# Kernel optimization log

Measured on AMD Instinct MI355X. Metric: run time of the kernel, lower is better.

The kernel has to match this reference:

```python
import jax, jax.numpy as jnp
import numpy as np

IN_SIZE = 5        # per-segment features: [number, In, former_number, speed0, speed1]
HIDDEN = 128
OUT_HIDDEN = 128
OUT_SIZE = 3       # input_size = output_size + 2 (structural constraint)
T_PREDICT = 4
B, T, S = 8, 128, 128


def setup_inputs() -> dict:
    key = jax.random.key(0)
    ks = jax.random.split(key, 5)
    scale = 0.05
    return {
        "input_data": jax.random.normal(ks[0], (B, T, S, IN_SIZE), jnp.float32),
        # seg_model: fused LSTM weight over concat(x, h, h_after, h_before)
        "W_cell": jax.random.normal(ks[1], (IN_SIZE + 3 * HIDDEN, 4 * HIDDEN), jnp.float32) * scale,
        "b_cell": jnp.zeros((4 * HIDDEN,), jnp.float32),
        # FCNet layerSize=[hidden, output_hidden, output]: Linear-ReLU-Linear
        "W1": jax.random.normal(ks[2], (HIDDEN, OUT_HIDDEN), jnp.float32) * scale,
        "b1": jnp.zeros((OUT_HIDDEN,), jnp.float32),
        "W2": jax.random.normal(ks[3], (OUT_HIDDEN, OUT_SIZE), jnp.float32) * scale,
        "b2": jnp.zeros((OUT_SIZE,), jnp.float32),
    }


def _cell(x, h, c, h_after, h_before, W, b):
    # LSTM cell on concat(x, h, h_after, h_before): [B,S,IN+3H] @ [IN+3H,4H]
    z = jnp.concatenate([x, h, h_after, h_before], axis=-1) @ W + b
    i, f, g, o = jnp.split(z, 4, axis=-1)
    c_new = jax.nn.sigmoid(f) * c + jax.nn.sigmoid(i) * jnp.tanh(g)
    h_new = jax.nn.sigmoid(o) * jnp.tanh(c_new)
    return h_new, c_new


def _next_input(former_input, next_input, output):
    # faithful translation of caculate_next_input
    speed_output = output[:, 1:, 1:]                    # [B,S-1,OUT-1]
    number_output = output[:, :, 0:1]                   # [B,S,1]
    speed_input = next_input[:, 0:1, 3:]                # [B,1,IN-3]
    In = jnp.concatenate([next_input[:, 0:1, 1:2], number_output[:, :-1, :]], axis=1)
    former_number = former_input[:, :, 2:3]
    number_caculate = former_number + In - number_output
    speed_next = jnp.concatenate([speed_input, speed_output], axis=1)
    return jnp.concatenate([number_output, In, number_caculate, speed_next], axis=2)


def reference(input_data, W_cell, b_cell, W1, b1, W2, b2):
    b, t, s, f = input_data.shape
    # time-major inputs for scan: x at time k and time k+1
    x_t = jnp.transpose(input_data[:, :-1], (1, 0, 2, 3))   # [T-1,B,S,F]
    x_tp1 = jnp.transpose(input_data[:, 1:], (1, 0, 2, 3))  # [T-1,B,S,F]
    h0 = jnp.zeros((b, s, HIDDEN), input_data.dtype)
    c0 = jnp.zeros((b, s, HIDDEN), input_data.dtype)

    def step(carry, xs):
        h, c = carry
        xt, xn = xs
        # spatial neighbor shift: h_after[i] = h[i+1], h_before[i] = h[i-1]
        h_after = jnp.pad(h[:, 1:, :], ((0, 0), (0, 1), (0, 0)))
        h_before = jnp.pad(h[:, :-1, :], ((0, 0), (1, 0), (0, 0)))
        h, c = _cell(xt, h, c, h_after, h_before, W_cell, b_cell)
        out = jnp.maximum(h @ W1 + b1, 0.0) @ W2 + b2
        nd = _next_input(xt, xn, out)
        return (h, c), nd

    _, nds = jax.lax.scan(step, (h0, c0), (x_t, x_tp1))     # [T-1,B,S,F]
    # original only writes outputs for time >= t_predict
    outputs = jnp.transpose(nds[T_PREDICT:], (1, 0, 2, 3))  # [B,T-TP-1,S,F]
    return outputs
```

## Files before the change

kernel.cpp:

```cpp
#include <hip/hip_runtime.h>
#include <hip/hip_bf16.h>


#define NB 8
#define NT 128
#define NS 128
#define NSTEP 127
#define TPRED 4
#define TOUT 123

typedef __attribute__((ext_vector_type(4))) float f32x4;
typedef __attribute__((ext_vector_type(8))) short s16x8;
typedef __attribute__((ext_vector_type(4))) unsigned int u32x4;

#define WS_WTC 0
#define WS_WT1 (512*384*2)
#define WS_PUB (WS_WT1 + 128*128*2)
#define WS_PUB_BYTES (2*8*8*2*128*4)

#define BARRIER() do { \
    __builtin_amdgcn_sched_barrier(0); \
    asm volatile("s_waitcnt lgkmcnt(0)" ::: "memory"); \
    __builtin_amdgcn_s_barrier(); \
    __builtin_amdgcn_sched_barrier(0); \
} while (0)

__device__ __forceinline__ unsigned swz(unsigned off) {
    return off ^ (((off >> 8) & 7u) << 4);
}

__global__ void init_weights(const float* __restrict__ Wc, const float* __restrict__ W1,
                             __hip_bfloat16* __restrict__ WTc, __hip_bfloat16* __restrict__ WT1)
{
    int i = blockIdx.x * blockDim.x + threadIdx.x;
    if (i < 512*384) {
        int cpp = i / 384, k = i % 384;
        int q = cpp >> 6, rem = cpp & 63, g = rem >> 4, h = rem & 15;
        int oc = g*128 + 16*q + h;
        int row = (k < 128) ? (261 + k) : ((k < 256) ? (5 + (k - 128)) : (133 + (k - 256)));
        WTc[cpp*384 + k] = __float2bfloat16(Wc[row*512 + oc]);
    } else {
        int qq = i - 512*384;
        if (qq < 128*128) {
            int nn = qq >> 7, k = qq & 127;
            WT1[nn*128 + k] = __float2bfloat16(W1[k*128 + nn]);
        }
    }
}

__global__ __launch_bounds__(512, 1) void lstm_persist(
    const float* __restrict__ input, const float* __restrict__ Wc,
    const float* __restrict__ bc, const float* __restrict__ b1v,
    const float* __restrict__ W2, const float* __restrict__ b2,
    float* __restrict__ outp,
    const __hip_bfloat16* __restrict__ WTc, const __hip_bfloat16* __restrict__ WT1,
    unsigned* pub)
{
    __shared__ __align__(16) __hip_bfloat16 hl[2*18*128];
    __shared__ __align__(16) __hip_bfloat16 relu_l[18*128];
    __shared__ float xl[3][80];
    __shared__ float outl[17*3];
    __shared__ float w2l[3*128];
    __shared__ float b2l[3];

    const int tid  = threadIdx.x;
    const int blk  = blockIdx.x;
    const int b    = blk & 7;
    const int c    = blk >> 3;
    const int lane = tid & 63;
    const int w    = tid >> 6;
    const int arow = lane & 15;
    const int kgrp = lane >> 4;
    const int hidw = 16*w + arow;

    for (int i = tid; i < 2*18*128; i += 512) ((unsigned short*)hl)[i] = 0;
    if (tid < 384) w2l[tid] = W2[(tid & 127)*3 + (tid >> 7)];
    if (tid >= 384 && tid < 387) b2l[tid - 384] = b2[tid - 384];

    float wxr[4][5], bcr[4];
    #pragma unroll
    for (int g = 0; g < 4; ++g) {
        const int cg = g*128 + hidw;
        bcr[g] = bc[cg];
        #pragma unroll
        for (int f = 0; f < 5; ++f) wxr[g][f] = Wc[f*512 + cg];
    }
    const float b1r = b1v[hidw];

    s16x8 brg[4][12];
    #pragma unroll
    for (int g = 0; g < 4; ++g)
        #pragma unroll
        for (int kt = 0; kt < 12; ++kt)
            brg[g][kt] = *(const s16x8*)((const char*)WTc +
                ((unsigned)(w*64 + g*16 + arow)*384 + kt*32 + kgrp*8)*2);
    s16x8 w1r[4];
    #pragma unroll
    for (int kt = 0; kt < 4; ++kt)
        w1r[kt] = *(const s16x8*)((const char*)WT1 + ((unsigned)(hidw)*128 + kt*32 + kgrp*8)*2);

    float cst[4] = {0.f, 0.f, 0.f, 0.f};

    if (tid < 80) xl[0][tid] = input[((unsigned)(b*NT)*NS + 16*c)*5 + tid];

    __syncthreads();

    for (int j = 0; j <= NSTEP; ++j) {
        const int jm3 = j % 3;
        const unsigned hlb  = (unsigned)(j & 1) * 4608u;
        const unsigned nhlb = (unsigned)((j + 1) & 1) * 4608u;

        if (j > 0 && tid < 64) {
            const bool left = (tid < 32);
            if (left ? (c > 0) : (c < 7)) {
                const unsigned jt = (unsigned)j;
                const int nc   = left ? (c - 1) : (c + 1);
                const int side = left ? 1 : 0;
                const int col4 = (tid & 31) * 4;
                const unsigned* q = pub + (unsigned)(((j & 1)*8 + b)*8 + nc)*256 + side*128 + col4;
                u32x4 g;
                for (;;) {
                    asm volatile("global_load_dwordx4 %0, %1, off sc0 sc1\n\ts_waitcnt vmcnt(0)"
                                 : "=v"(g) : "v"(q) : "memory");
                    if ((g[0] >> 16) == jt && (g[1] >> 16) == jt &&
                        (g[2] >> 16) == jt && (g[3] >> 16) == jt) break;
                }
                __builtin_amdgcn_sched_barrier(0);
                const unsigned long long pk =
                    (unsigned long long)(g[0] & 0xffffu)        |
                    ((unsigned long long)(g[1] & 0xffffu) << 16) |
                    ((unsigned long long)(g[2] & 0xffffu) << 32) |
                    ((unsigned long long)(g[3] & 0xffffu) << 48);
                const int row = left ? 0 : 17;
                *(unsigned long long*)((char*)hl + hlb + swz((unsigned)(row*256 + col4*2))) = pk;
            }
        }
        float xr = 0.f;
        const bool xact = (j < NSTEP) && (tid < 80);
        if (xact) xr = input[((unsigned)(b*NT + j + 1)*NS + 16*c)*5 + tid];

        BARRIER();

        if (j < NSTEP) {
            f32x4 a0 = {0.f,0.f,0.f,0.f}, a1 = a0, a2 = a0, a3 = a0;
            const unsigned ab = (unsigned)(arow*256 + kgrp*16);
            #pragma unroll
            for (int kt = 0; kt < 4; ++kt) {
                const s16x8 av = *(const s16x8*)((const char*)hl + hlb + swz(ab + kt*64));
                a0 = __builtin_amdgcn_mfma_f32_16x16x32_bf16(av, brg[0][kt], a0, 0, 0, 0);
                a1 = __builtin_amdgcn_mfma_f32_16x16x32_bf16(av, brg[1][kt], a1, 0, 0, 0);
                a2 = __builtin_amdgcn_mfma_f32_16x16x32_bf16(av, brg[2][kt], a2, 0, 0, 0);
                a3 = __builtin_amdgcn_mfma_f32_16x16x32_bf16(av, brg[3][kt], a3, 0, 0, 0);
            }
            #pragma unroll
            for (int kt = 4; kt < 8; ++kt) {
                const s16x8 av = *(const s16x8*)((const char*)hl + hlb + swz(ab + 256 + (kt-4)*64));
                a0 = __builtin_amdgcn_mfma_f32_16x16x32_bf16(av, brg[0][kt], a0, 0, 0, 0);
                a1 = __builtin_amdgcn_mfma_f32_16x16x32_bf16(av, brg[1][kt], a1, 0, 0, 0);
                a2 = __builtin_amdgcn_mfma_f32_16x16x32_bf16(av, brg[2][kt], a2, 0, 0, 0);
                a3 = __builtin_amdgcn_mfma_f32_16x16x32_bf16(av, brg[3][kt], a3, 0, 0, 0);
            }
            #pragma unroll
            for (int kt = 8; kt < 12; ++kt) {
                const s16x8 av = *(const s16x8*)((const char*)hl + hlb + swz(ab + 512 + (kt-8)*64));
                a0 = __builtin_amdgcn_mfma_f32_16x16x32_bf16(av, brg[0][kt], a0, 0, 0, 0);
                a1 = __builtin_amdgcn_mfma_f32_16x16x32_bf16(av, brg[1][kt], a1, 0, 0, 0);
                a2 = __builtin_amdgcn_mfma_f32_16x16x32_bf16(av, brg[2][kt], a2, 0, 0, 0);
                a3 = __builtin_amdgcn_mfma_f32_16x16x32_bf16(av, brg[3][kt], a3, 0, 0, 0);
            }
            asm volatile("s_waitcnt vmcnt(0)" ::: "memory");
            unsigned short h0b = 0, h3b = 0;
            #pragma unroll
            for (int r = 0; r < 4; ++r) {
                const int lr0 = kgrp*4 + r;
                const float xv0 = xl[jm3][lr0*5+0], xv1 = xl[jm3][lr0*5+1], xv2 = xl[jm3][lr0*5+2],
                            xv3 = xl[jm3][lr0*5+3], xv4 = xl[jm3][lr0*5+4];
                const float iv = a0[r] + bcr[0] + xv0*wxr[0][0] + xv1*wxr[0][1] + xv2*wxr[0][2] + xv3*wxr[0][3] + xv4*wxr[0][4];
                const float fv = a1[r] + bcr[1] + xv0*wxr[1][0] + xv1*wxr[1][1] + xv2*wxr[1][2] + xv3*wxr[1][3] + xv4*wxr[1][4];
                const float gv = a2[r] + bcr[2] + xv0*wxr[2][0] + xv1*wxr[2][1] + xv2*wxr[2][2] + xv3*wxr[2][3] + xv4*wxr[2][4];
                const float ov = a3[r] + bcr[3] + xv0*wxr[3][0] + xv1*wxr[3][1] + xv2*wxr[3][2] + xv3*wxr[3][3] + xv4*wxr[3][4];
                const float si = __builtin_amdgcn_rcpf(1.f + __expf(-iv));
                const float sf = __builtin_amdgcn_rcpf(1.f + __expf(-fv));
                const float so = __builtin_amdgcn_rcpf(1.f + __expf(-ov));
                const float tg = 1.f - 2.f*__builtin_amdgcn_rcpf(__expf(2.f*gv) + 1.f);
                const float cn = sf*cst[r] + si*tg;
                cst[r] = cn;
                const float tc = 1.f - 2.f*__builtin_amdgcn_rcpf(__expf(2.f*cn) + 1.f);
                const float hn = so*tc;
                __hip_bfloat16 hbv = __float2bfloat16(hn);
                const unsigned short hbits = *(const unsigned short*)&hbv;
                *(unsigned short*)((char*)hl + nhlb + swz((unsigned)((lr0 + 1)*256 + hidw*2))) = hbits;
                if (r == 0) h0b = hbits;
                if (r == 3) h3b = hbits;
            }
            unsigned* pbase = pub + (unsigned)((((j+1) & 1)*8 + b)*8 + c)*256;
            const unsigned jt1 = (unsigned)(j + 1) << 16;
            if (c > 0 && kgrp == 0)
                asm volatile("global_store_dword %0, %1, off sc0 sc1"
                             :: "v"(pbase + hidw), "v"(jt1 | (unsigned)h0b) : "memory");
            if (c < 7 && kgrp == 3)
                asm volatile("global_store_dword %0, %1, off sc0 sc1"
                             :: "v"(pbase + 128 + hidw), "v"(jt1 | (unsigned)h3b) : "memory");
        }

        if (j >= TPRED + 1) {
            const int jm1_3 = (j - 1) % 3;
            f32x4 c0 = {0.f,0.f,0.f,0.f}, c1 = c0;
            const unsigned w1a = (unsigned)(arow*256 + kgrp*16);
            #pragma unroll
            for (int kt = 0; kt < 4; ++kt) {
                const s16x8 av0 = *(const s16x8*)((const char*)hl + hlb + swz(w1a + kt*64));
                const s16x8 av1 = *(const s16x8*)((const char*)hl + hlb + swz(w1a + 256 + kt*64));
                c0 = __builtin_amdgcn_mfma_f32_16x16x32_bf16(av0, w1r[kt], c0, 0, 0, 0);
                c1 = __builtin_amdgcn_mfma_f32_16x16x32_bf16(av1, w1r[kt], c1, 0, 0, 0);
            }
            #pragma unroll
            for (int r = 0; r < 4; ++r) {
                const int lr = kgrp*4 + r;
                const float v0 = fmaxf(c0[r] + b1r, 0.f);
                *(__hip_bfloat16*)((char*)relu_l + swz((unsigned)(lr*256 + hidw*2))) = __float2bfloat16(v0);
                if (lr == 15) {
                    const float v1 = fmaxf(c1[r] + b1r, 0.f);
                    *(__hip_bfloat16*)((char*)relu_l + swz((unsigned)(16*256 + hidw*2))) = __float2bfloat16(v1);
                }
            }
            BARRIER();
            if (tid < 51) {
                const int m = tid / 3, p = tid - m*3;
                float s = b2l[p];
                #pragma unroll
                for (int kc = 0; kc < 16; ++kc) {
                    union { s16x8 v; unsigned short u[8]; } uu;
                    uu.v = *(const s16x8*)((const char*)relu_l + swz((unsigned)(m*256 + kc*16)));
                    #pragma unroll
                    for (int e = 0; e < 8; ++e)
                        s += __uint_as_float((unsigned)uu.u[e] << 16) * w2l[p*128 + kc*8 + e];
                }
                outl[m*3 + p] = s;
            }
            if (tid < 16) {
                const int m = tid, grow = 16*c + m;
                const float no = outl[(m + 1)*3 + 0];
                float In, sp0, sp1;
                if (m == 0 && c == 0) { In = xl[jm3][1]; sp0 = xl[jm3][3]; sp1 = xl[jm3][4]; }
                else { In = outl[m*3 + 0]; sp0 = outl[(m + 1)*3 + 1]; sp1 = outl[(m + 1)*3 + 2]; }
                const float former = xl[jm1_3][m*5 + 2];
                const long base = ((long)(b*TOUT + (j - 1 - TPRED))*NS + grow)*5;
                outp[base + 0] = no;
                outp[base + 1] = In;
                outp[base + 2] = former + In - no;
                outp[base + 3] = sp0;
                outp[base + 4] = sp1;
            }
        }

        if (xact) xl[(j + 1) % 3][tid] = xr;
    }
}

extern "C" void kernel_launch(void* const* d_in, const int* in_sizes, int n_in,
                              void* d_out, int out_size, void* d_ws, size_t ws_size,
                              hipStream_t stream) {
    const float* input = (const float*)d_in[0];
    const float* Wc    = (const float*)d_in[1];
    const float* bc    = (const float*)d_in[2];
    const float* W1    = (const float*)d_in[3];
    const float* b1    = (const float*)d_in[4];
    const float* W2    = (const float*)d_in[5];
    const float* b2    = (const float*)d_in[6];
    float* outp = (float*)d_out;
    char* ws = (char*)d_ws;

    __hip_bfloat16* WTc = (__hip_bfloat16*)(ws + WS_WTC);
    __hip_bfloat16* WT1 = (__hip_bfloat16*)(ws + WS_WT1);
    unsigned*       pub = (unsigned*)(ws + WS_PUB);

    hipMemsetAsync(ws + WS_PUB, 0, WS_PUB_BYTES, stream);
    init_weights<<<832, 256, 0, stream>>>(Wc, W1, WTc, WT1);
    lstm_persist<<<64, 512, 0, stream>>>(input, Wc, bc, b1, W2, b2, outp, WTc, WT1, pub);
}
```

Baseline: 1.003 ms.

## Exchange halos every 8 steps using 8-row ghost zones with redundant compute

Each block now computes 32 rows per step: its own 16 plus 8 ghost rows on each side. Neighbour h and c state is exchanged through global memory only every 8 steps instead of every step. The input projection and bias are folded into the MFMA as extra K columns, fed from a bf16 input tile with a ones column and weights held in LDS. This trades double the MFMA and gate work per step for far fewer inter-block spin-waits, and it adds LDS pressure.

```diff
diff --git a/kernel.cpp b/kernel.cpp
--- a/kernel.cpp
+++ b/kernel.cpp
@@ -14,9 +14,9 @@
 typedef __attribute__((ext_vector_type(4))) unsigned int u32x4;
 
 #define WS_WTC 0
-#define WS_WT1 (512*384*2)
-#define WS_PUB (WS_WT1 + 128*128*2)
-#define WS_PUB_BYTES (2*8*8*2*128*4)
+#define WS_WT1 (512*416*2)
+#define WS_HCP (WS_WT1 + 128*128*2)
+#define WS_HCP_BYTES (2*8*8*2*8*128*8)
 
 #define BARRIER() do { \
     __builtin_amdgcn_sched_barrier(0); \
@@ -29,35 +29,41 @@
     return off ^ (((off >> 8) & 7u) << 4);
 }
 
-__global__ void init_weights(const float* __restrict__ Wc, const float* __restrict__ W1,
+__global__ void init_weights(const float* __restrict__ Wc, const float* __restrict__ bc,
+                             const float* __restrict__ W1,
                              __hip_bfloat16* __restrict__ WTc, __hip_bfloat16* __restrict__ WT1)
 {
     int i = blockIdx.x * blockDim.x + threadIdx.x;
-    if (i < 512*384) {
-        int cpp = i / 384, k = i % 384;
+    if (i < 512*416) {
+        int cpp = i / 416, k = i % 416;
         int q = cpp >> 6, rem = cpp & 63, g = rem >> 4, h = rem & 15;
         int oc = g*128 + 16*q + h;
-        int row = (k < 128) ? (261 + k) : ((k < 256) ? (5 + (k - 128)) : (133 + (k - 256)));
-        WTc[cpp*384 + k] = __float2bfloat16(Wc[row*512 + oc]);
-    } else {
-        int qq = i - 512*384;
-        if (qq < 128*128) {
-            int nn = qq >> 7, k = qq & 127;
-            WT1[nn*128 + k] = __float2bfloat16(W1[k*128 + nn]);
-        }
+        float v;
+        if      (k < 128) v = Wc[(261 + k)*512 + oc];
+        else if (k < 256) v = Wc[(5 + (k - 128))*512 + oc];
+        else if (k < 384) v = Wc[(133 + (k - 256))*512 + oc];
+        else if (k < 389) v = Wc[(k - 384)*512 + oc];
+        else if (k == 389) v = bc[oc];
+        else v = 0.f;
+        WTc[cpp*416 + k] = __float2bfloat16(v);
+    } else if (i < 512*416 + 128*128) {
+        int qq = i - 512*416;
+        int nn = qq >> 7, k = qq & 127;
+        WT1[nn*128 + k] = __float2bfloat16(W1[k*128 + nn]);
     }
 }
 
 __global__ __launch_bounds__(512, 1) void lstm_persist(
-    const float* __restrict__ input, const float* __restrict__ Wc,
-    const float* __restrict__ bc, const float* __restrict__ b1v,
+    const float* __restrict__ input, const float* __restrict__ b1v,
     const float* __restrict__ W2, const float* __restrict__ b2,
     float* __restrict__ outp,
     const __hip_bfloat16* __restrict__ WTc, const __hip_bfloat16* __restrict__ WT1,
-    unsigned* pub)
+    unsigned long long* hcpub)
 {
-    __shared__ __align__(16) __hip_bfloat16 hl[2*18*128];
+    __shared__ __align__(16) __hip_bfloat16 hl[2*34*128];
+    __shared__ __align__(16) __hip_bfloat16 bl[512*104];
     __shared__ __align__(16) __hip_bfloat16 relu_l[18*128];
+    __shared__ __align__(16) __hip_bfloat16 xlt[2*32*40];
     __shared__ float xl[3][80];
     __shared__ float outl[17*3];
     __shared__ float w2l[3*128];
@@ -67,146 +73,237 @@
     const int blk  = blockIdx.x;
     const int b    = blk & 7;
     const int c    = blk >> 3;
+    const int s0   = 16*c;
     const int lane = tid & 63;
-    const int w    = tid >> 6;
+    const int q    = tid >> 6;
     const int arow = lane & 15;
     const int kgrp = lane >> 4;
-    const int hidw = 16*w + arow;
-
-    for (int i = tid; i < 2*18*128; i += 512) ((unsigned short*)hl)[i] = 0;
+    const int hidw = 16*q + arow;
+
+    for (int i = tid; i < 2*34*128; i += 512) ((unsigned short*)hl)[i] = 0;
+    for (int i = tid; i < 2*32*40; i += 512) ((unsigned short*)xlt)[i] = 0;
     if (tid < 384) w2l[tid] = W2[(tid & 127)*3 + (tid >> 7)];
     if (tid >= 384 && tid < 387) b2l[tid - 384] = b2[tid - 384];
-
-    float wxr[4][5], bcr[4];
-    #pragma unroll
-    for (int g = 0; g < 4; ++g) {
-        const int cg = g*128 + hidw;
-        bcr[g] = bc[cg];
-        #pragma unroll
-        for (int f = 0; f < 5; ++f) wxr[g][f] = Wc[f*512 + cg];
+    for (int i = tid; i < 512*24; i += 512) {
+        const int col = i / 24, r8 = i % 24;
+        const int kt = 10 + (r8 >> 3), sub = r8 & 7;
+        *(unsigned long long*)((char*)bl + col*208 + (kt - 10)*64 + sub*8) =
+            *(const unsigned long long*)((const char*)WTc + ((unsigned)col*416 + kt*32 + sub*4)*2);
     }
-    const float b1r = b1v[hidw];
-
-    s16x8 brg[4][12];
+    if (tid < 80) xl[0][tid] = input[((unsigned)(b*NT)*NS + s0)*5 + tid];
+    if (tid < 32) {
+        int g = s0 - 8 + tid; g = g < 0 ? 0 : (g > 127 ? 127 : g);
+        const float* xp = input + ((unsigned)(b*NT)*NS + g)*5;
+        unsigned short* xr0 = (unsigned short*)((char*)xlt + tid*80);
+        __hip_bfloat16 v0 = __float2bfloat16(xp[0]), v1 = __float2bfloat16(xp[1]),
+                       v2 = __float2bfloat16(xp[2]), v3 = __float2bfloat16(xp[3]),
+                       v4 = __float2bfloat16(xp[4]);
+        xr0[0] = *(unsigned short*)&v0; xr0[1] = *(unsigned short*)&v1;
+        xr0[2] = *(unsigned short*)&v2; xr0[3] = *(unsigned short*)&v3;
+        xr0[4] = *(unsigned short*)&v4; xr0[5] = 0x3F80;
+    }
+
+    s16x8 brg[4][10];
     #pragma unroll
     for (int g = 0; g < 4; ++g)
         #pragma unroll
-        for (int kt = 0; kt < 12; ++kt)
+        for (int kt = 0; kt < 10; ++kt)
             brg[g][kt] = *(const s16x8*)((const char*)WTc +
-                ((unsigned)(w*64 + g*16 + arow)*384 + kt*32 + kgrp*8)*2);
+                ((unsigned)(q*64 + g*16 + arow)*416 + kt*32 + kgrp*8)*2);
     s16x8 w1r[4];
     #pragma unroll
     for (int kt = 0; kt < 4; ++kt)
-        w1r[kt] = *(const s16x8*)((const char*)WT1 + ((unsigned)(hidw)*128 + kt*32 + kgrp*8)*2);
-
-    float cst[4] = {0.f, 0.f, 0.f, 0.f};
-
-    if (tid < 80) xl[0][tid] = input[((unsigned)(b*NT)*NS + 16*c)*5 + tid];
+        w1r[kt] = *(const s16x8*)((const char*)WT1 + ((unsigned)hidw*128 + kt*32 + kgrp*8)*2);
+    const float b1r = b1v[hidw];
+
+    float cst[8];
+    #pragma unroll
+    for (int i = 0; i < 8; ++i) cst[i] = 0.f;
 
     __syncthreads();
 
     for (int j = 0; j <= NSTEP; ++j) {
         const int jm3 = j % 3;
-        const unsigned hlb  = (unsigned)(j & 1) * 4608u;
-        const unsigned nhlb = (unsigned)((j + 1) & 1) * 4608u;
-
-        if (j > 0 && tid < 64) {
-            const bool left = (tid < 32);
-            if (left ? (c > 0) : (c < 7)) {
-                const unsigned jt = (unsigned)j;
-                const int nc   = left ? (c - 1) : (c + 1);
-                const int side = left ? 1 : 0;
-                const int col4 = (tid & 31) * 4;
-                const unsigned* q = pub + (unsigned)(((j & 1)*8 + b)*8 + nc)*256 + side*128 + col4;
-                u32x4 g;
+        const unsigned hlb  = (unsigned)(j & 1) * 8704u;
+        const unsigned nhlb = (unsigned)((j + 1) & 1) * 8704u;
+        const unsigned xlb  = (unsigned)(j & 1) * 2560u;
+
+        float xr = 0.f, p0 = 0.f, p1 = 0.f, p2 = 0.f, p3 = 0.f, p4 = 0.f;
+        const bool act80 = (j < NSTEP) && (tid < 80);
+        const bool act32 = (j < NSTEP) && (tid < 32);
+        if (act80) xr = input[((unsigned)(b*NT + j + 1)*NS + s0)*5 + tid];
+        if (act32) {
+            int g = s0 - 8 + tid; g = g < 0 ? 0 : (g > 127 ? 127 : g);
+            const float* xp = input + ((unsigned)(b*NT + j + 1)*NS + g)*5;
+            p0 = xp[0]; p1 = xp[1]; p2 = xp[2]; p3 = xp[3]; p4 = xp[4];
+        }
+
+        const bool isgather = (j > 0) && ((j & 7) == 0);
+        if (isgather) {
+            const unsigned wtag = (unsigned)(j >> 3);
+            const unsigned par  = wtag & 1;
+            const int side = tid >> 8;
+            const int i2   = tid & 255;
+            const bool act = (side == 0) ? (c > 0) : (c < 7);
+            if (act) {
+                const int nc = (side == 0) ? c - 1 : c + 1;
+                const int ns = 1 - side;
+                const unsigned long long* qp =
+                    hcpub + (unsigned)((((par*8 + b)*8 + nc)*2 + ns)*1024 + i2*4);
+                u32x4 ga, gb;
                 for (;;) {
-                    asm volatile("global_load_dwordx4 %0, %1, off sc0 sc1\n\ts_waitcnt vmcnt(0)"
-                                 : "=v"(g) : "v"(q) : "memory");
-                    if ((g[0] >> 16) == jt && (g[1] >> 16) == jt &&
-                        (g[2] >> 16) == jt && (g[3] >> 16) == jt) break;
+                    asm volatile(
+                        "global_load_dwordx4 %0, %2, off sc0 sc1\n\t"
+                        "global_load_dwordx4 %1, %3, off sc0 sc1\n\t"
+                        "s_waitcnt vmcnt(0)"
+                        : "=&v"(ga), "=&v"(gb)
+                        : "v"(qp), "v"(qp + 2) : "memory");
+                    if ((ga[1] >> 16) == wtag && (ga[3] >> 16) == wtag &&
+                        (gb[1] >> 16) == wtag && (gb[3] >> 16) == wtag) break;
                 }
                 __builtin_amdgcn_sched_barrier(0);
+                const int row = i2 >> 5, col0 = (i2 & 31)*4;
+                const int lr = (side == 0) ? 1 + row : 25 + row;
                 const unsigned long long pk =
-                    (unsigned long long)(g[0] & 0xffffu)        |
-                    ((unsigned long long)(g[1] & 0xffffu) << 16) |
-                    ((unsigned long long)(g[2] & 0xffffu) << 32) |
-                    ((unsigned long long)(g[3] & 0xffffu) << 48);
-                const int row = left ? 0 : 17;
-                *(unsigned long long*)((char*)hl + hlb + swz((unsigned)(row*256 + col4*2))) = pk;
-            }
-        }
-        float xr = 0.f;
-        const bool xact = (j < NSTEP) && (tid < 80);
-        if (xact) xr = input[((unsigned)(b*NT + j + 1)*NS + 16*c)*5 + tid];
-
+                    (unsigned long long)(ga[1] & 0xffffu)
+                  | ((unsigned long long)(ga[3] & 0xffffu) << 16)
+                  | ((unsigned long long)(gb[1] & 0xffffu) << 32)
+                  | ((unsigned long long)(gb[3] & 0xffffu) << 48);
+                *(unsigned long long*)((char*)hl + hlb + swz((unsigned)(lr*256 + col0*2))) = pk;
+            }
+            BARRIER();
+            if (c > 0 && kgrp < 2) {
+                const unsigned long long* cp =
+                    hcpub + (unsigned)((((par*8 + b)*8 + (c - 1))*2 + 1)*1024 + (kgrp*4)*128 + hidw);
+                unsigned long long v0, v1, v2, v3;
+                asm volatile(
+                    "global_load_dwordx2 %0, %4, off sc0 sc1\n\t"
+                    "global_load_dwordx2 %1, %5, off sc0 sc1\n\t"
+                    "global_load_dwordx2 %2, %6, off sc0 sc1\n\t"
+                    "global_load_dwordx2 %3, %7, off sc0 sc1\n\t"
+                    "s_waitcnt vmcnt(0)"
+                    : "=&v"(v0), "=&v"(v1), "=&v"(v2), "=&v"(v3)
+                    : "v"(cp), "v"(cp + 128), "v"(cp + 256), "v"(cp + 384) : "memory");
+                cst[0] = __uint_as_float((unsigned)v0);
+                cst[1] = __uint_as_float((unsigned)v1);
+                cst[2] = __uint_as_float((unsigned)v2);
+                cst[3] = __uint_as_float((unsigned)v3);
+            }
+            if (c < 7 && kgrp >= 2) {
+                const unsigned long long* cp =
+                    hcpub + (unsigned)((((par*8 + b)*8 + (c + 1))*2 + 0)*1024 + ((kgrp - 2)*4)*128 + hidw);
+                unsigned long long v0, v1, v2, v3;
+                asm volatile(
+                    "global_load_dwordx2 %0, %4, off sc0 sc1\n\t"
+                    "global_load_dwordx2 %1, %5, off sc0 sc1\n\t"
+                    "global_load_dwordx2 %2, %6, off sc0 sc1\n\t"
+                    "global_load_dwordx2 %3, %7, off sc0 sc1\n\t"
+                    "s_waitcnt vmcnt(0)"
+                    : "=&v"(v0), "=&v"(v1), "=&v"(v2), "=&v"(v3)
+                    : "v"(cp), "v"(cp + 128), "v"(cp + 256), "v"(cp + 384) : "memory");
+                cst[4] = __uint_as_float((unsigned)v0);
+                cst[5] = __uint_as_float((unsigned)v1);
+                cst[6] = __uint_as_float((unsigned)v2);
+                cst[7] = __uint_as_float((unsigned)v3);
+            }
+        }
         BARRIER();
 
         if (j < NSTEP) {
-            f32x4 a0 = {0.f,0.f,0.f,0.f}, a1 = a0, a2 = a0, a3 = a0;
-            const unsigned ab = (unsigned)(arow*256 + kgrp*16);
+            const bool PUB = ((j + 1) & 7) == 0;
+            const unsigned wtag1 = (unsigned)((j + 1) >> 3);
+            unsigned hsv[4], csv[4];
             #pragma unroll
-            for (int kt = 0; kt < 4; ++kt) {
-                const s16x8 av = *(const s16x8*)((const char*)hl + hlb + swz(ab + kt*64));
-                a0 = __builtin_amdgcn_mfma_f32_16x16x32_bf16(av, brg[0][kt], a0, 0, 0, 0);
-                a1 = __builtin_amdgcn_mfma_f32_16x16x32_bf16(av, brg[1][kt], a1, 0, 0, 0);
-                a2 = __builtin_amdgcn_mfma_f32_16x16x32_bf16(av, brg[2][kt], a2, 0, 0, 0);
-                a3 = __builtin_amdgcn_mfma_f32_16x16x32_bf16(av, brg[3][kt], a3, 0, 0, 0);
-            }
-            #pragma unroll
-            for (int kt = 4; kt < 8; ++kt) {
-                const s16x8 av = *(const s16x8*)((const char*)hl + hlb + swz(ab + 256 + (kt-4)*64));
-                a0 = __builtin_amdgcn_mfma_f32_16x16x32_bf16(av, brg[0][kt], a0, 0, 0, 0);
-                a1 = __builtin_amdgcn_mfma_f32_16x16x32_bf16(av, brg[1][kt], a1, 0, 0, 0);
-                a2 = __builtin_amdgcn_mfma_f32_16x16x32_bf16(av, brg[2][kt], a2, 0, 0, 0);
-                a3 = __builtin_amdgcn_mfma_f32_16x16x32_bf16(av, brg[3][kt], a3, 0, 0, 0);
-            }
-            #pragma unroll
-            for (int kt = 8; kt < 12; ++kt) {
-                const s16x8 av = *(const s16x8*)((const char*)hl + hlb + swz(ab + 512 + (kt-8)*64));
-                a0 = __builtin_amdgcn_mfma_f32_16x16x32_bf16(av, brg[0][kt], a0, 0, 0, 0);
-                a1 = __builtin_amdgcn_mfma_f32_16x16x32_bf16(av, brg[1][kt], a1, 0, 0, 0);
-                a2 = __builtin_amdgcn_mfma_f32_16x16x32_bf16(av, brg[2][kt], a2, 0, 0, 0);
-                a3 = __builtin_amdgcn_mfma_f32_16x16x32_bf16(av, brg[3][kt], a3, 0, 0, 0);
-            }
-            asm volatile("s_waitcnt vmcnt(0)" ::: "memory");
-            unsigned short h0b = 0, h3b = 0;
-            #pragma unroll
-            for (int r = 0; r < 4; ++r) {
-                const int lr0 = kgrp*4 + r;
-                const float xv0 = xl[jm3][lr0*5+0], xv1 = xl[jm3][lr0*5+1], xv2 = xl[jm3][lr0*5+2],
-                            xv3 = xl[jm3][lr0*5+3], xv4 = xl[jm3][lr0*5+4];
-                const float iv = a0[r] + bcr[0] + xv0*wxr[0][0] + xv1*wxr[0][1] + xv2*wxr[0][2] + xv3*wxr[0][3] + xv4*wxr[0][4];
-                const float fv = a1[r] + bcr[1] + xv0*wxr[1][0] + xv1*wxr[1][1] + xv2*wxr[1][2] + xv3*wxr[1][3] + xv4*wxr[1][4];
-                const float gv = a2[r] + bcr[2] + xv0*wxr[2][0] + xv1*wxr[2][1] + xv2*wxr[2][2] + xv3*wxr[2][3] + xv4*wxr[2][4];
-                const float ov = a3[r] + bcr[3] + xv0*wxr[3][0] + xv1*wxr[3][1] + xv2*wxr[3][2] + xv3*wxr[3][3] + xv4*wxr[3][4];
-                const float si = __builtin_amdgcn_rcpf(1.f + __expf(-iv));
-                const float sf = __builtin_amdgcn_rcpf(1.f + __expf(-fv));
-                const float so = __builtin_amdgcn_rcpf(1.f + __expf(-ov));
-                const float tg = 1.f - 2.f*__builtin_amdgcn_rcpf(__expf(2.f*gv) + 1.f);
-                const float cn = sf*cst[r] + si*tg;
-                cst[r] = cn;
-                const float tc = 1.f - 2.f*__builtin_amdgcn_rcpf(__expf(2.f*cn) + 1.f);
-                const float hn = so*tc;
-                __hip_bfloat16 hbv = __float2bfloat16(hn);
-                const unsigned short hbits = *(const unsigned short*)&hbv;
-                *(unsigned short*)((char*)hl + nhlb + swz((unsigned)((lr0 + 1)*256 + hidw*2))) = hbits;
-                if (r == 0) h0b = hbits;
-                if (r == 3) h3b = hbits;
-            }
-            unsigned* pbase = pub + (unsigned)((((j+1) & 1)*8 + b)*8 + c)*256;
-            const unsigned jt1 = (unsigned)(j + 1) << 16;
-            if (c > 0 && kgrp == 0)
-                asm volatile("global_store_dword %0, %1, off sc0 sc1"
-                             :: "v"(pbase + hidw), "v"(jt1 | (unsigned)h0b) : "memory");
-            if (c < 7 && kgrp == 3)
-                asm volatile("global_store_dword %0, %1, off sc0 sc1"
-                             :: "v"(pbase + 128 + hidw), "v"(jt1 | (unsigned)h3b) : "memory");
+            for (int mt = 0; mt < 2; ++mt) {
+                f32x4 a0 = {0.f,0.f,0.f,0.f}, a1 = a0, a2 = a0, a3 = a0;
+                const unsigned ab = (unsigned)((mt*16 + arow)*256 + kgrp*16);
+                #pragma unroll
+                for (int kt = 0; kt < 4; ++kt) {
+                    const s16x8 av = *(const s16x8*)((const char*)hl + hlb + swz(ab + kt*64));
+                    a0 = __builtin_amdgcn_mfma_f32_16x16x32_bf16(av, brg[0][kt], a0, 0, 0, 0);
+                    a1 = __builtin_amdgcn_mfma_f32_16x16x32_bf16(av, brg[1][kt], a1, 0, 0, 0);
+                    a2 = __builtin_amdgcn_mfma_f32_16x16x32_bf16(av, brg[2][kt], a2, 0, 0, 0);
+                    a3 = __builtin_amdgcn_mfma_f32_16x16x32_bf16(av, brg[3][kt], a3, 0, 0, 0);
+                }
+                #pragma unroll
+                for (int kt = 4; kt < 8; ++kt) {
+                    const s16x8 av = *(const s16x8*)((const char*)hl + hlb + swz(ab + 256 + (kt-4)*64));
+                    a0 = __builtin_amdgcn_mfma_f32_16x16x32_bf16(av, brg[0][kt], a0, 0, 0, 0);
+                    a1 = __builtin_amdgcn_mfma_f32_16x16x32_bf16(av, brg[1][kt], a1, 0, 0, 0);
+                    a2 = __builtin_amdgcn_mfma_f32_16x16x32_bf16(av, brg[2][kt], a2, 0, 0, 0);
+                    a3 = __builtin_amdgcn_mfma_f32_16x16x32_bf16(av, brg[3][kt], a3, 0, 0, 0);
+                }
+                #pragma unroll
+                for (int kt = 8; kt < 10; ++kt) {
+                    const s16x8 av = *(const s16x8*)((const char*)hl + hlb + swz(ab + 512 + (kt-8)*64));
+                    a0 = __builtin_amdgcn_mfma_f32_16x16x32_bf16(av, brg[0][kt], a0, 0, 0, 0);
+                    a1 = __builtin_amdgcn_mfma_f32_16x16x32_bf16(av, brg[1][kt], a1, 0, 0, 0);
+                    a2 = __builtin_amdgcn_mfma_f32_16x16x32_bf16(av, brg[2][kt], a2, 0, 0, 0);
+                    a3 = __builtin_amdgcn_mfma_f32_16x16x32_bf16(av, brg[3][kt], a3, 0, 0, 0);
+                }
+                #pragma unroll
+                for (int kt = 10; kt < 12; ++kt) {
+                    const s16x8 av = *(const s16x8*)((const char*)hl + hlb + swz(ab + 512 + (kt-8)*64));
+                    const char* blb = (const char*)bl + (kt - 10)*64 + kgrp*16;
+                    a0 = __builtin_amdgcn_mfma_f32_16x16x32_bf16(av, *(const s16x8*)(blb + (q*64 + 0*16 + arow)*208), a0, 0, 0, 0);
+                    a1 = __builtin_amdgcn_mfma_f32_16x16x32_bf16(av, *(const s16x8*)(blb + (q*64 + 1*16 + arow)*208), a1, 0, 0, 0);
+                    a2 = __builtin_amdgcn_mfma_f32_16x16x32_bf16(av, *(const s16x8*)(blb + (q*64 + 2*16 + arow)*208), a2, 0, 0, 0);
+                    a3 = __builtin_amdgcn_mfma_f32_16x16x32_bf16(av, *(const s16x8*)(blb + (q*64 + 3*16 + arow)*208), a3, 0, 0, 0);
+                }
+                {
+                    const s16x8 av = *(const s16x8*)((const char*)xlt + xlb +
+                                                     (unsigned)((mt*16 + arow)*80 + kgrp*16));
+                    const char* blb = (const char*)bl + 128 + kgrp*16;
+                    a0 = __builtin_amdgcn_mfma_f32_16x16x32_bf16(av, *(const s16x8*)(blb + (q*64 + 0*16 + arow)*208), a0, 0, 0, 0);
+                    a1 = __builtin_amdgcn_mfma_f32_16x16x32_bf16(av, *(const s16x8*)(blb + (q*64 + 1*16 + arow)*208), a1, 0, 0, 0);
+                    a2 = __builtin_amdgcn_mfma_f32_16x16x32_bf16(av, *(const s16x8*)(blb + (q*64 + 2*16 + arow)*208), a2, 0, 0, 0);
+                    a3 = __builtin_amdgcn_mfma_f32_16x16x32_bf16(av, *(const s16x8*)(blb + (q*64 + 3*16 + arow)*208), a3, 0, 0, 0);
+                }
+                #pragma unroll
+                for (int r = 0; r < 4; ++r) {
+                    const int trow = mt*16 + kgrp*4 + r;
+                    const int g    = s0 - 8 + trow;
+                    const float si = __builtin_amdgcn_rcpf(1.f + __expf(-a0[r]));
+                    const float sf = __builtin_amdgcn_rcpf(1.f + __expf(-a1[r]));
+                    const float so = __builtin_amdgcn_rcpf(1.f + __expf(-a3[r]));
+                    const float tg = 1.f - 2.f*__builtin_amdgcn_rcpf(__expf(2.f*a2[r]) + 1.f);
+                    const float cn = sf*cst[mt*4 + r] + si*tg;
+                    cst[mt*4 + r] = cn;
+                    const float tc = 1.f - 2.f*__builtin_amdgcn_rcpf(__expf(2.f*cn) + 1.f);
+                    const float hn = so*tc;
+                    __hip_bfloat16 hbv = __float2bfloat16(hn);
+                    const unsigned short hbits = *(const unsigned short*)&hbv;
+                    if ((unsigned)g < 128u)
+                        *(unsigned short*)((char*)hl + nhlb +
+                            swz((unsigned)((trow + 1)*256 + hidw*2))) = hbits;
+                    if (PUB && ((mt == 0) == (kgrp >= 2))) {
+                        hsv[r] = (unsigned)hbits;
+                        csv[r] = __float_as_uint(cn);
+                    }
+                }
+            }
+            if (PUB) {
+                const unsigned par1 = wtag1 & 1;
+                const int side  = (kgrp >= 2) ? 0 : 1;
+                const int prow0 = (kgrp >= 2) ? (kgrp - 2)*4 : kgrp*4;
+                unsigned long long* pb =
+                    hcpub + (unsigned)((((par1*8 + b)*8 + c)*2 + side)*1024 + hidw);
+                #pragma unroll
+                for (int r = 0; r < 4; ++r) {
+                    const unsigned long long word =
+                        ((unsigned long long)wtag1 << 48)
+                      | ((unsigned long long)hsv[r] << 32)
+                      | (unsigned long long)csv[r];
+                    asm volatile("global_store_dwordx2 %0, %1, off sc0 sc1"
+                                 :: "v"(pb + (prow0 + r)*128), "v"(word) : "memory");
+                }
+            }
         }
 
         if (j >= TPRED + 1) {
             const int jm1_3 = (j - 1) % 3;
             f32x4 c0 = {0.f,0.f,0.f,0.f}, c1 = c0;
-            const unsigned w1a = (unsigned)(arow*256 + kgrp*16);
+            const unsigned w1a = (unsigned)((8 + arow)*256 + kgrp*16);
             #pragma unroll
             for (int kt = 0; kt < 4; ++kt) {
                 const s16x8 av0 = *(const s16x8*)((const char*)hl + hlb + swz(w1a + kt*64));
@@ -239,7 +336,7 @@
                 outl[m*3 + p] = s;
             }
             if (tid < 16) {
-                const int m = tid, grow = 16*c + m;
+                const int m = tid, grow = s0 + m;
                 const float no = outl[(m + 1)*3 + 0];
                 float In, sp0, sp1;
                 if (m == 0 && c == 0) { In = xl[jm3][1]; sp0 = xl[jm3][3]; sp1 = xl[jm3][4]; }
@@ -254,7 +351,17 @@
             }
         }
 
-        if (xact) xl[(j + 1) % 3][tid] = xr;
+        if (act80) xl[(j + 1) % 3][tid] = xr;
+        if (act32) {
+            __hip_bfloat16 v0 = __float2bfloat16(p0), v1 = __float2bfloat16(p1),
+                           v2 = __float2bfloat16(p2), v3 = __float2bfloat16(p3),
+                           v4 = __float2bfloat16(p4);
+            unsigned short* xr0 = (unsigned short*)((char*)xlt +
+                (unsigned)((j + 1) & 1)*2560u + tid*80);
+            xr0[0] = *(unsigned short*)&v0; xr0[1] = *(unsigned short*)&v1;
+            xr0[2] = *(unsigned short*)&v2; xr0[3] = *(unsigned short*)&v3;
+            xr0[4] = *(unsigned short*)&v4; xr0[5] = 0x3F80;
+        }
     }
 }
 
@@ -273,9 +380,9 @@
 
     __hip_bfloat16* WTc = (__hip_bfloat16*)(ws + WS_WTC);
     __hip_bfloat16* WT1 = (__hip_bfloat16*)(ws + WS_WT1);
-    unsigned*       pub = (unsigned*)(ws + WS_PUB);
-
-    hipMemsetAsync(ws + WS_PUB, 0, WS_PUB_BYTES, stream);
-    init_weights<<<832, 256, 0, stream>>>(Wc, W1, WTc, WT1);
-    lstm_persist<<<64, 512, 0, stream>>>(input, Wc, bc, b1, W2, b2, outp, WTc, WT1, pub);
+    unsigned long long* hcp = (unsigned long long*)(ws + WS_HCP);
+
+    hipMemsetAsync(ws + WS_HCP, 0, WS_HCP_BYTES, stream);
+    init_weights<<<896, 256, 0, stream>>>(Wc, bc, W1, WTc, WT1);
+    lstm_persist<<<64, 512, 0, stream>>>(input, b1, W2, b2, outp, WTc, WT1, hcp);
 }
```

After: 1.415 ms. 41.1% more time.
